# Kernel tuning notes

Measured on AMD Instinct MI355X. Metric: run time of the kernel, lower is better.

Reference implementation:

```python
import jax, jax.numpy as jnp
import numpy as np

B, H, W, D, C, K, ITERS = 16, 64, 64, 64, 16, 5, 4
EPS_LN = 1e-5

def _ln(x, g, b):
    m = x.mean(-1, keepdims=True)
    v = jnp.mean((x - m) ** 2, axis=-1, keepdims=True)
    return (x - m) / jnp.sqrt(v + EPS_LN) * g + b

def _build_grid(h, w):
    # (h, w, 2) with x in [-1,1] over width, y in [-1,1] over height
    y, x = jnp.meshgrid(jnp.linspace(-1.0, 1.0, h), jnp.linspace(-1.0, 1.0, w), indexing='ij')
    return jnp.stack([x, y], axis=-1)

def _forward(feat, feat_color, mask, slot_noise, slots_mu, slots_logsigma,
             w_grid, b_grid, w_k, w_v, ln_kv_g, ln_kv_b, w_mlp, b_mlp,
             ln_q_g, ln_q_b, w_q, w_ih, w_hh, b_ih, b_hh,
             ln_feat_g, ln_feat_b, ln_color_g, ln_color_b,
             ln_res_g, ln_res_b, w_res, b_res):
    b, h, w, d = feat.shape
    n = h * w
    k_slots = mask.shape[0]
    scale = d ** (-0.5)

    grid = _build_grid(h, w)  # (H, W, 2)

    # fg position: weighted mean of grid under mask -> (K, 2), broadcast to (B, K, 2)
    gm = grid.transpose(2, 0, 1)[None] * mask            # (K, 2, H, W)
    fg_pos = gm.sum((2, 3)) / (mask.sum((2, 3)) + 1e-5)  # (K, 2)
    fg_pos = jnp.broadcast_to(fg_pos[None], (b, k_slots, 2))

    feat_n = _ln(feat.reshape(b, n, d), ln_feat_g, ln_feat_b)                    # (B, N, D)
    featc_n = _ln(feat_color.reshape(b, n, feat_color.shape[-1]), ln_color_g, ln_color_b)

    slot = slots_mu + jnp.exp(slots_logsigma) * slot_noise  # (B, K, D)

    # k/v with relative positional grid embedding (fg_pos is constant across iters,
    # so k/v are iteration-invariant and computed once -- same math as the original loop)
    rel = grid[None, None] - fg_pos[:, :, None, None, :]        # (B, K, H, W, 2)
    rel4 = jnp.concatenate([rel, -rel], -1).reshape(b, k_slots, n, 4)
    grid_embed = rel4 @ w_grid.T + b_grid                       # (B, K, N, D)
    k = _ln(feat_n @ w_k.T[None] [0][None][0][None][0] if False else (feat_n @ w_k.T)[:, None] + grid_embed, ln_kv_g, ln_kv_b) @ w_mlp.T + b_mlp
    v = _ln((feat_n @ w_v.T)[:, None] + grid_embed, ln_kv_g, ln_kv_b) @ w_mlp.T + b_mlp

    attn = None
    for it in range(ITERS):
        prev = slot
        q = _ln(slot, ln_q_g, ln_q_b) @ w_q.T                         # (B, K, D)
        logits = jnp.einsum('bkd,bknd->bkn', q, k) * scale
        attn = jax.nn.softmax(logits, axis=-1)                        # (B, K, N)
        upd = jnp.einsum('bkn,bknd->bkd', attn, v)                    # (B, K, D)
        if it != ITERS - 1:
            # torch GRUCell
            x = upd.reshape(-1, d)
            hp = slot.reshape(-1, d)
            gi = x @ w_ih.T + b_ih
            gh = hp @ w_hh.T + b_hh
            i_r, i_z, i_n = jnp.split(gi, 3, axis=-1)
            h_r, h_z, h_n = jnp.split(gh, 3, axis=-1)
            r = jax.nn.sigmoid(i_r + h_r)
            z = jax.nn.sigmoid(i_z + h_z)
            nn_ = jnp.tanh(i_n + r * h_n)
            slot = ((1.0 - z) * nn_ + z * hp).reshape(b, k_slots, d)
            slot = _ln(slot, ln_res_g, ln_res_b) @ w_res.T + b_res + prev
        else:
            slot_color = jnp.einsum('bkn,bnc->bkc', attn, featc_n)
            slot = jnp.concatenate([slot, slot_color], axis=-1)       # (B, K, D+C)

    amin = attn.min(axis=2, keepdims=True)
    amax = attn.max(axis=2, keepdims=True)
    attn = (attn - amin) / (amax - amin + 1e-5)
    return slot, fg_pos, attn

def setup_inputs() -> dict:
    key = jax.random.key(0)
    ks = jax.random.split(key, 16)
    def rn(i, shape, s=0.02):
        return jax.random.normal(ks[i], shape, jnp.float32) * s
    return {
        'feat': jax.random.normal(ks[0], (B, H, W, D), jnp.float32),
        'feat_color': jax.random.normal(ks[1], (B, H, W, C), jnp.float32),
        'mask': jax.random.uniform(ks[2], (K, 1, H, W), jnp.float32),
        'slot_noise': jax.random.normal(ks[3], (B, K, D), jnp.float32),
        'slots_mu': rn(4, (1, 1, D), 1.0),
        'slots_logsigma': rn(5, (1, 1, D), 0.01),
        'w_grid': rn(6, (D, 4)), 'b_grid': jnp.zeros((D,), jnp.float32),
        'w_k': rn(7, (D, D)), 'w_v': rn(8, (D, D)),
        'ln_kv_g': jnp.ones((D,), jnp.float32), 'ln_kv_b': jnp.zeros((D,), jnp.float32),
        'w_mlp': rn(9, (D, D)), 'b_mlp': jnp.zeros((D,), jnp.float32),
        'ln_q_g': jnp.ones((D,), jnp.float32), 'ln_q_b': jnp.zeros((D,), jnp.float32),
        'w_q': rn(10, (D, D)),
        'w_ih': rn(11, (3 * D, D)), 'w_hh': rn(12, (3 * D, D)),
        'b_ih': jnp.zeros((3 * D,), jnp.float32), 'b_hh': jnp.zeros((3 * D,), jnp.float32),
        'ln_feat_g': jnp.ones((D,), jnp.float32), 'ln_feat_b': jnp.zeros((D,), jnp.float32),
        'ln_color_g': jnp.ones((C,), jnp.float32), 'ln_color_b': jnp.zeros((C,), jnp.float32),
        'ln_res_g': jnp.ones((D,), jnp.float32), 'ln_res_b': jnp.zeros((D,), jnp.float32),
        'w_res': rn(13, (D, D)), 'b_res': jnp.zeros((D,), jnp.float32),
    }

def reference(feat, feat_color, mask, slot_noise, slots_mu, slots_logsigma,
              w_grid, b_grid, w_k, w_v, ln_kv_g, ln_kv_b, w_mlp, b_mlp,
              ln_q_g, ln_q_b, w_q, w_ih, w_hh, b_ih, b_hh,
              ln_feat_g, ln_feat_b, ln_color_g, ln_color_b,
              ln_res_g, ln_res_b, w_res, b_res):
    return _forward(feat, feat_color, mask, slot_noise, slots_mu, slots_logsigma,
                    w_grid, b_grid, w_k, w_v, ln_kv_g, ln_kv_b, w_mlp, b_mlp,
                    ln_q_g, ln_q_b, w_q, w_ih, w_hh, b_ih, b_hh,
                    ln_feat_g, ln_feat_b, ln_color_g, ln_color_b,
                    ln_res_g, ln_res_b, w_res, b_res)
```

## Files before the change

kernel.cpp:

```cpp
#include <hip/hip_runtime.h>
#include <stdint.h>

#define B_ 16
#define H_ 64
#define W_ 64
#define D_ 64
#define C_ 16
#define K_ 5
#define N_ 4096
#define NC_ 16
#define CS_ 256
#define EPS 1e-5f

typedef __attribute__((ext_vector_type(8))) short bf16x8;
typedef __attribute__((ext_vector_type(4))) float f32x4;

__device__ __forceinline__ float wsum64(float v){
  #pragma unroll
  for(int o=1;o<64;o<<=1) v += __shfl_xor(v,o,64);
  return v;
}
__device__ __forceinline__ float wmax64(float v){
  #pragma unroll
  for(int o=1;o<64;o<<=1) v = fmaxf(v, __shfl_xor(v,o,64));
  return v;
}
__device__ __forceinline__ float wmin64(float v){
  #pragma unroll
  for(int o=1;o<64;o<<=1) v = fminf(v, __shfl_xor(v,o,64));
  return v;
}
__device__ __forceinline__ uint16_t f2bf(float f){
  uint32_t u = __float_as_uint(f);
  u += 0x7fffu + ((u>>16)&1u);
  return (uint16_t)(u>>16);
}

__global__ __launch_bounds__(256) void k_pre(
    const float* __restrict__ mask, const float* __restrict__ noise,
    const float* __restrict__ mu, const float* __restrict__ lsg,
    const float* __restrict__ wm, const float* __restrict__ bm, const float* __restrict__ lnkb,
    const float* __restrict__ wk, const float* __restrict__ wv, const float* __restrict__ lnfb,
    const float* __restrict__ wq, const float* __restrict__ lnqg, const float* __restrict__ lnqb,
    const float* __restrict__ wres, const float* __restrict__ bres,
    const float* __restrict__ lnrg, const float* __restrict__ lnrb,
    const float* __restrict__ wih, const float* __restrict__ whh,
    const float* __restrict__ wg, const float* __restrict__ bg,
    float* __restrict__ ws_fg, float* __restrict__ out_fg,
    float* __restrict__ bm2, float* __restrict__ fkb, float* __restrict__ fvb,
    float* __restrict__ qb, float* __restrict__ br2,
    float* __restrict__ wgx, float* __restrict__ wgy, float* __restrict__ gscal,
    float* __restrict__ wqpT, float* __restrict__ wrpT,
    float* __restrict__ wvT, float* __restrict__ wmT,
    float* __restrict__ gw, float* __restrict__ slot){
  int bid=blockIdx.x, tid=threadIdx.x;
  if(bid<5){
    int k=bid;
    float sm=0.f, sx=0.f, sy=0.f;
    for(int p=tid; p<H_*W_; p+=256){
      int i=p>>6, j=p&63;
      float m = mask[k*H_*W_ + p];
      float x = -1.f + (2.f/63.f)*j;
      float y = -1.f + (2.f/63.f)*i;
      sm+=m; sx+=m*x; sy+=m*y;
    }
    __shared__ float r0[4], r1[4], r2[4];
    int wid=tid>>6, lane=tid&63;
    sm=wsum64(sm); sx=wsum64(sx); sy=wsum64(sy);
    if(lane==0){ r0[wid]=sm; r1[wid]=sx; r2[wid]=sy; }
    __syncthreads();
    if(tid==0){
      float tm=r0[0]+r0[1]+r0[2]+r0[3];
      float tx=r1[0]+r1[1]+r1[2]+r1[3];
      float ty=r2[0]+r2[1]+r2[2]+r2[3];
      float px = tx/(tm+1e-5f), py = ty/(tm+1e-5f);
      ws_fg[k*2+0]=px; ws_fg[k*2+1]=py;
      for(int b=0;b<B_;b++){ out_fg[(b*K_+k)*2+0]=px; out_fg[(b*K_+k)*2+1]=py; }
    }
  } else if(bid==5){
    int sel=tid>>6, o=tid&63; float s=0.f;
    if(sel==0){ s=bm[o]; for(int d=0;d<64;d++) s+=lnkb[d]*wm[o*64+d]; bm2[o]=s; }
    else if(sel==1){ for(int d=0;d<64;d++) s+=lnqb[d]*wq[o*64+d]; qb[o]=0.125f*s; }
    else if(sel==2){ for(int d=0;d<64;d++) s+=lnrb[d]*wres[o*64+d]; br2[o]=s+bres[o]; }
    else { for(int d=0;d<64;d++) s+=lnfb[d]*wk[o*64+d]; fkb[o]=s; }
  } else if(bid==6){
    int wv4=tid>>6, l=tid&63;
    if(wv4==0){ float s=0.f; for(int d=0;d<64;d++) s+=lnfb[d]*wv[l*64+d]; fvb[l]=s; }
    else if(wv4==1){
      float4 w4 = *(const float4*)(wg + l*4);
      wgx[l]=w4.x-w4.z; wgy[l]=w4.y-w4.w;
    } else if(wv4==2){
      float4 w4 = *(const float4*)(wg + l*4);
      float wx=w4.x-w4.z, wy=w4.y-w4.w, bl=bg[l];
      float t;
      t=wsum64(wx);    if(l==0) gscal[0]=t*(1.f/64.f);
      t=wsum64(wy);    if(l==0) gscal[1]=t*(1.f/64.f);
      t=wsum64(bl);    if(l==0) gscal[2]=t*(1.f/64.f);
      t=wsum64(wx*wx); if(l==0) gscal[3]=t*(1.f/64.f);
      t=wsum64(wy*wy); if(l==0) gscal[4]=t*(1.f/64.f);
      t=wsum64(wx*wy); if(l==0) gscal[5]=t*(2.f/64.f);
      t=wsum64(wx*bl); if(l==0) gscal[6]=t*(2.f/64.f);
      t=wsum64(wy*bl); if(l==0) gscal[7]=t*(2.f/64.f);
      t=wsum64(bl*bl); if(l==0) gscal[8]=t*(1.f/64.f);
    }
  } else if(bid<71){
    int i=(bid-7)*256+tid;
    int a=i>>12, r=i&4095, d=r>>6, o=r&63;
    if(a==0)      wqpT[r]=0.125f*lnqg[d]*wq[o*64+d];
    else if(a==1) wrpT[r]=lnrg[d]*wres[o*64+d];
    else if(a==2) wvT[r]=wv[o*64+d];
    else          wmT[r]=wm[o*64+d];
  } else if(bid<167){
    int i=(bid-71)*256+tid;
    int g6=i>>12, r=i&4095, d=r>>6, o=r&63;
    float v = (g6<3)? wih[(g6*64+o)*64+d] : whh[((g6-3)*64+o)*64+d];
    gw[g6*4096 + d*64 + o] = v;
  } else {
    int i=(bid-167)*256+tid;
    if(i<B_*K_*D_){ int d=i&63; slot[i]=mu[d]+expf(lsg[d])*noise[i]; }
  }
}

__global__ __launch_bounds__(256) void k_featln(const float* __restrict__ feat,
    const float* __restrict__ wk, const float* __restrict__ wv, const float* __restrict__ gf,
    const float* __restrict__ fkb, const float* __restrict__ fvb,
    const float* __restrict__ wgx, const float* __restrict__ wgy, const float* __restrict__ bg,
    const float* __restrict__ fc, const float* __restrict__ gc, const float* __restrict__ bc,
    uint16_t* __restrict__ Aout, float4* __restrict__ kstat, float4* __restrict__ vstat,
    float* __restrict__ fcn){
  int tid=threadIdx.x, wid=tid>>6, lane=tid&63;
  int q=lane>>4, c=lane&15;
  size_t row = (size_t)blockIdx.x*64 + wid*16 + c;
  const float* xp = feat + row*64;
  float x[16];
  *(float4*)&x[0]  = *(const float4*)(xp + q*8);
  *(float4*)&x[4]  = *(const float4*)(xp + q*8 + 4);
  *(float4*)&x[8]  = *(const float4*)(xp + 32 + q*8);
  *(float4*)&x[12] = *(const float4*)(xp + 36 + q*8);
  float s=0.f;
  #pragma unroll
  for(int i=0;i<16;i++) s+=x[i];
  s += __shfl_xor(s,16,64); s += __shfl_xor(s,32,64);
  float mean = s*(1.f/64.f);
  float v=0.f;
  #pragma unroll
  for(int i=0;i<16;i++){ float d=x[i]-mean; v+=d*d; }
  v += __shfl_xor(v,16,64); v += __shfl_xor(v,32,64);
  float rs = rsqrtf(v*(1.f/64.f)+EPS);
  float gl[16];
  *(float4*)&gl[0]  = *(const float4*)(gf + q*8);
  *(float4*)&gl[4]  = *(const float4*)(gf + q*8 + 4);
  *(float4*)&gl[8]  = *(const float4*)(gf + 32 + q*8);
  *(float4*)&gl[12] = *(const float4*)(gf + 36 + q*8);
  bf16x8 A0, A1;
  #pragma unroll
  for(int j=0;j<8;j++){
    A0[j] = (short)f2bf((x[j]  -mean)*rs);
    A1[j] = (short)f2bf((x[8+j]-mean)*rs);
  }
  *(bf16x8*)(Aout + row*64 + q*8) = A0;
  *(bf16x8*)(Aout + row*64 + 32 + q*8) = A1;
  float wgxl[4][4], wgyl[4][4], bgl[4][4];
  #pragma unroll
  for(int ot=0;ot<4;ot++){
    *(float4*)&wgxl[ot][0] = *(const float4*)(wgx + ot*16 + q*4);
    *(float4*)&wgyl[ot][0] = *(const float4*)(wgy + ot*16 + q*4);
    *(float4*)&bgl[ot][0]  = *(const float4*)(bg + ot*16 + q*4);
  }
  #pragma unroll
  for(int mat=0;mat<2;mat++){
    const float* w = mat? wv : wk;
    const float* fb = mat? fvb : fkb;
    float ss=0.f, s2=0.f, dx=0.f, dy=0.f, db=0.f;
    #pragma unroll
    for(int ot=0; ot<4; ot++){
      const float* wp = w + (size_t)(ot*16+c)*64 + q*8;
      bf16x8 W0, W1;
      #pragma unroll
      for(int j=0;j<8;j++){ W0[j]=(short)f2bf(wp[j]*gl[j]); W1[j]=(short)f2bf(wp[32+j]*gl[8+j]); }
      float4 bq = *(const float4*)(fb + ot*16 + q*4);
      f32x4 acc = {bq.x,bq.y,bq.z,bq.w};
      acc = __builtin_amdgcn_mfma_f32_16x16x32_bf16(W0, A0, acc, 0,0,0);
      acc = __builtin_amdgcn_mfma_f32_16x16x32_bf16(W1, A1, acc, 0,0,0);
      #pragma unroll
      for(int r=0;r<4;r++){
        float a=acc[r];
        ss+=a; s2+=a*a;
        dx = fmaf(a, wgxl[ot][r], dx);
        dy = fmaf(a, wgyl[ot][r], dy);
        db = fmaf(a, bgl[ot][r], db);
      }
    }
    ss += __shfl_xor(ss,16,64); ss += __shfl_xor(ss,32,64);
    s2 += __shfl_xor(s2,16,64); s2 += __shfl_xor(s2,32,64);
    dx += __shfl_xor(dx,16,64); dx += __shfl_xor(dx,32,64);
    dy += __shfl_xor(dy,16,64); dy += __shfl_xor(dy,32,64);
    db += __shfl_xor(db,16,64); db += __shfl_xor(db,32,64);
    if(lane<16){
      size_t row2 = (size_t)blockIdx.x*64 + wid*16 + lane;
      float4 st = { ss*(1.f/64.f), s2*(1.f/64.f)+db*(1.f/32.f), dx*(1.f/32.f), dy*(1.f/32.f) };
      (mat? vstat : kstat)[row2] = st;
    }
  }
  int r16=tid>>4, cc=tid&15;
  #pragma unroll
  for(int i=0;i<4;i++){
    size_t row2 = (size_t)blockIdx.x*64 + i*16 + r16;
    float xv = fc[row2*16+cc];
    float sc=xv;
    #pragma unroll
    for(int o=1;o<16;o<<=1) sc += __shfl_xor(sc,o,16);
    float m2 = sc*(1.f/16.f);
    float df = xv-m2;
    float v2 = df*df;
    #pragma unroll
    for(int o=1;o<16;o<<=1) v2 += __shfl_xor(v2,o,16);
    fcn[row2*16+cc] = df*rsqrtf(v2*(1.f/16.f)+EPS)*gc[cc] + bc[cc];
  }
}

template<bool GRU>
__global__ __launch_bounds__(256) void k_slotq(
    const float* __restrict__ slot_prev, float* __restrict__ slot_cur,
    const float* __restrict__ part, const float* __restrict__ pscal,
    const float* __restrict__ red_in,
    const float* __restrict__ gw,
    const float* __restrict__ bih, const float* __restrict__ bhh,
    const float* __restrict__ wrpT, const float* __restrict__ br2,
    const float* __restrict__ wqpT, const float* __restrict__ qb,
    const float* __restrict__ wm, const float* __restrict__ wk,
    const float* __restrict__ lnfg, const float* __restrict__ lnkg,
    const float* __restrict__ fkb, const float* __restrict__ bm2, const float* __restrict__ fvb,
    const float* __restrict__ wvT, const float* __restrict__ wmT,
    const float* __restrict__ wgx, const float* __restrict__ wgy, const float* __restrict__ bg,
    const float* __restrict__ gscal,
    float* __restrict__ qs_out, float* __restrict__ cst_out){
  __shared__ float vv[64], vh[64];
  __shared__ float red6[4][64][6];
  int bk=blockIdx.x;
  int tid=threadIdx.x, wid=tid>>6, lane=tid&63;
  int o=lane, qq=wid;
  float mwgx=gscal[0], mwgy=gscal[1], mbg=gscal[2];

  #define MV(Wptr) { float p_=0.f; \
      _Pragma("unroll") \
      for(int dd=0;dd<16;dd++) p_ = fmaf(vv[qq*16+dd], (Wptr)[(qq*16+dd)*64+o], p_); \
      red6[qq][o][0]=p_; } __syncthreads();
  #define SUM0 (red6[0][lane][0]+red6[1][lane][0]+red6[2][lane][0]+red6[3][lane][0])

  float cur=0.f, qv=0.f, qp=0.f, hp=0.f;
  if(GRU){
    float As=0.f, Ax=0.f, Ay=0.f, Am=0.f;
    if(wid==0){
      float mred[NC_], sred[NC_];
      #pragma unroll
      for(int cc=0;cc<NC_;cc++){
        const float* rp = red_in + ((size_t)bk*NC_+cc)*4;
        mred[cc]=rp[0]; sred[cc]=rp[1];
      }
      float M=-1e30f;
      #pragma unroll
      for(int cc=0;cc<NC_;cc++) M=fmaxf(M,mred[cc]);
      float S=0.f;
      #pragma unroll
      for(int cc=0;cc<NC_;cc++){ mred[cc]=__expf(mred[cc]-M); S=fmaf(sred[cc],mred[cc],S); }
      float invS=1.f/S;
      float sA=0.f;
      #pragma unroll
      for(int cc=0;cc<NC_;cc++){
        float lam = mred[cc]*invS;
        sA = fmaf(lam, part[((size_t)bk*NC_+cc)*64+lane], sA);
        const float* pp = pscal + ((size_t)bk*NC_+cc)*4;
        As=fmaf(lam,pp[0],As); Ax=fmaf(lam,pp[1],Ax);
        Ay=fmaf(lam,pp[2],Ay); Am=fmaf(lam,pp[3],Am);
      }
      vv[lane] = lnfg[lane]*sA;
    }
    __syncthreads();
    MV(wvT);
    if(wid==0){
      float fvs = SUM0 + fvb[lane]*As;
      float zs = fvs + Ax*wgx[lane] + Ay*wgy[lane] + As*bg[lane] - Am;
      vv[lane] = lnkg[lane]*zs;
    }
    __syncthreads();
    MV(wmT);
    if(wid==0){
      float x_ = SUM0 + bm2[lane];
      hp = slot_prev[bk*64+lane];
      vv[lane]=x_; vh[lane]=hp;
    }
    __syncthreads();
    {
      float p0=0.f,p1=0.f,p2=0.f,p3=0.f,p4=0.f,p5=0.f;
      #pragma unroll
      for(int dd=0;dd<16;dd++){
        int d = qq*16+dd;
        float xd=vv[d], hd=vh[d];
        p0 = fmaf(xd, gw[d*64+o], p0);
        p1 = fmaf(xd, gw[4096+d*64+o], p1);
        p2 = fmaf(xd, gw[8192+d*64+o], p2);
        p3 = fmaf(hd, gw[12288+d*64+o], p3);
        p4 = fmaf(hd, gw[16384+d*64+o], p4);
        p5 = fmaf(hd, gw[20480+d*64+o], p5);
      }
      red6[qq][o][0]=p0; red6[qq][o][1]=p1; red6[qq][o][2]=p2;
      red6[qq][o][3]=p3; red6[qq][o][4]=p4; red6[qq][o][5]=p5;
    }
    __syncthreads();
    if(wid==0){
      float gir=bih[lane], giz=bih[64+lane], gin=bih[128+lane];
      float ghr=bhh[lane], ghz=bhh[64+lane], ghn=bhh[128+lane];
      #pragma unroll
      for(int w=0;w<4;w++){
        gir+=red6[w][lane][0]; giz+=red6[w][lane][1]; gin+=red6[w][lane][2];
        ghr+=red6[w][lane][3]; ghz+=red6[w][lane][4]; ghn+=red6[w][lane][5];
      }
      float r=1.f/(1.f+__expf(-(gir+ghr)));
      float z=1.f/(1.f+__expf(-(giz+ghz)));
      float nn=tanhf(gin+r*ghn);
      float sp=(1.f-z)*nn+z*hp;
      float m=wsum64(sp)*(1.f/64.f); float df=sp-m;
      float var=wsum64(df*df)*(1.f/64.f);
      vv[lane]=df*rsqrtf(var+EPS);
    }
    __syncthreads();
    MV(wrpT);
    if(wid==0){
      cur = SUM0 + br2[lane] + hp;
      slot_cur[bk*64+lane]=cur;
    }
  } else {
    if(wid==0) cur = slot_prev[bk*64+lane];
  }
  __syncthreads();
  if(wid==0){
    float m=wsum64(cur)*(1.f/64.f); float df=cur-m;
    float var=wsum64(df*df)*(1.f/64.f);
    vv[lane]=df*rsqrtf(var+EPS);
  }
  __syncthreads();
  MV(wqpT);
  if(wid==0){ qv = SUM0 + qb[lane]; vv[lane]=qv; }
  __syncthreads();
  MV(wm);
  if(wid==0){ qp = SUM0*lnkg[lane]; vv[lane]=qp; }
  __syncthreads();
  MV(wk);
  if(wid==0){
    qs_out[bk*64+lane] = SUM0*lnfg[lane];
    float s1 = wsum64(qp);
    float c1 = wsum64(qp*wgx[lane]);
    float c2 = wsum64(qp*wgy[lane]);
    float c3 = wsum64(qp*(bg[lane]+fkb[lane]));
    float c4c = wsum64(qv*bm2[lane]);
    if(lane==0){
      float* cp = cst_out + bk*8;
      cp[0]=c1-s1*mwgx; cp[1]=c2-s1*mwgy; cp[2]=c3-s1*mbg; cp[3]=s1; cp[4]=c4c;
    }
  }
  #undef MV
  #undef SUM0
}

template<bool FINAL>
__global__ __launch_bounds__(256) void k_attn(const uint16_t* __restrict__ Aw,
    const float4* __restrict__ kstat, const float4* __restrict__ vstat,
    const float* __restrict__ qsg, const float* __restrict__ cstg,
    const float* __restrict__ gscal, const float* __restrict__ ws_fg,
    float* __restrict__ lgt, float* __restrict__ red_out,
    float* __restrict__ part_o, float* __restrict__ pscal_o){
  __shared__ uint32_t As_[CS_*32];
  __shared__ float dps[5][CS_+1];
  __shared__ float pw[4][5][64];
  __shared__ float rm[4], rn[4];
  __shared__ float rsc[4][5];
  __shared__ float cstl[5][5];
  __shared__ float fgl[5][2];
  int chunk=blockIdx.x, b=blockIdx.y;
  int tid=threadIdx.x, wid=tid>>6, lane=tid&63;
  int c=lane&15, q=lane>>4;
  float mwgx=gscal[0], mwgy=gscal[1], mbg=gscal[2];
  float g1=gscal[3], g2=gscal[4], g3=gscal[5], g4=gscal[6], g5=gscal[7], g6=gscal[8];

  const uint4* Ag = (const uint4*)(Aw + ((size_t)b*N_ + chunk*CS_)*64);
  #pragma unroll
  for(int jj=0;jj<8;jj++){
    int f = jj*256 + tid;
    uint4 u = Ag[f];
    *(uint4*)(As_ + f*4) = u;
  }
  if(tid<25) cstl[tid/5][tid%5] = cstg[(b*K_ + tid/5)*8 + (tid%5)];
  if(tid>=32 && tid<42){ int i2=tid-32; fgl[i2>>1][i2&1] = ws_fg[i2]; }
  __syncthreads();

  {
    bf16x8 QF0={0,0,0,0,0,0,0,0}, QF1={0,0,0,0,0,0,0,0};
    if(c<5){
      const float* qpp = qsg + (b*K_+c)*64;
      #pragma unroll
      for(int j=0;j<8;j++){
        QF0[j] = (short)f2bf(qpp[q*8+j]);
        QF1[j] = (short)f2bf(qpp[32+q*8+j]);
      }
    }
    const uint16_t* Abase = Aw + ((size_t)b*N_ + chunk*CS_)*64;
    #pragma unroll
    for(int it=0;it<4;it++){
      int tile = wid*64 + it*16;
      const uint16_t* rp = Abase + (size_t)(tile+c)*64;
      bf16x8 BF0 = *(const bf16x8*)(rp + q*8);
      bf16x8 BF1 = *(const bf16x8*)(rp + 32 + q*8);
      f32x4 acc = {0.f,0.f,0.f,0.f};
      acc = __builtin_amdgcn_mfma_f32_16x16x32_bf16(QF0, BF0, acc, 0,0,0);
      acc = __builtin_amdgcn_mfma_f32_16x16x32_bf16(QF1, BF1, acc, 0,0,0);
      #pragma unroll
      for(int r=0;r<4;r++){
        int s = q*4+r;
        if(s<5) dps[s][tile+c]=acc[r];
      }
    }
  }
  __syncthreads();

  int t = tid;
  int n = chunk*CS_ + t;
  float4 st = kstat[(size_t)b*N_ + n];
  float4 sv;
  if(!FINAL) sv = vstat[(size_t)b*N_ + n];
  float gx = -1.f + (2.f/63.f)*(n&63);
  float gy = -1.f + (2.f/63.f)*(n>>6);
  #pragma unroll
  for(int k=0;k<5;k++){
    float rx = gx - fgl[k][0], ry = gy - fgl[k][1];
    float CX=cstl[k][0], CY=cstl[k][1], C0=cstl[k][2], S1=cstl[k][3], C4=cstl[k][4];
    float quad = g1*rx*rx + g2*ry*ry + g3*rx*ry + g4*rx + g5*ry + g6;
    float mu = st.x + rx*mwgx + ry*mwgy + mbg;
    float var = st.y + rx*st.z + ry*st.w + quad - mu*mu;
    float rsn = rsqrtf(var+EPS);
    float l = rsn*(dps[k][t] + rx*CX + ry*CY + C0 - S1*st.x) + C4;
    float wmx = wmax64(l);
    if(lane==0) rm[wid]=wmx;
    if(FINAL){ float mn=wmin64(l); if(lane==0) rn[wid]=mn; }
    __syncthreads();
    float m_c = fmaxf(fmaxf(rm[0],rm[1]),fmaxf(rm[2],rm[3]));
    float e = __expf(l-m_c);
    float scq=e, As2=0.f, Ax2=0.f, Ay2=0.f, Am2=0.f, w_=0.f;
    if(!FINAL){
      float muV = sv.x + rx*mwgx + ry*mwgy + mbg;
      float varV = sv.y + rx*sv.z + ry*sv.w + quad - muV*muV;
      float rsv_ = rsqrtf(varV+EPS);
      w_ = e*rsv_;
      As2=w_; Ax2=w_*rx; Ay2=w_*ry; Am2=w_*muV;
    } else {
      lgt[(size_t)(b*K_+k)*N_ + n] = l;
    }
    scq=wsum64(scq);
    if(!FINAL){ As2=wsum64(As2); Ax2=wsum64(Ax2); Ay2=wsum64(Ay2); Am2=wsum64(Am2); }
    if(lane==0){ rsc[wid][0]=scq; rsc[wid][1]=As2; rsc[wid][2]=Ax2; rsc[wid][3]=Ay2; rsc[wid][4]=Am2; }
    __syncthreads();
    if(tid==0){
      size_t idx = ((size_t)(b*K_+k)*NC_+chunk)*4;
      red_out[idx+0]=m_c;
      red_out[idx+1]=rsc[0][0]+rsc[1][0]+rsc[2][0]+rsc[3][0];
      if(FINAL) red_out[idx+2]=fminf(fminf(rn[0],rn[1]),fminf(rn[2],rn[3]));
      if(!FINAL){
        pscal_o[idx+0]=rsc[0][1]+rsc[1][1]+rsc[2][1]+rsc[3][1];
        pscal_o[idx+1]=rsc[0][2]+rsc[1][2]+rsc[2][2]+rsc[3][2];
        pscal_o[idx+2]=rsc[0][3]+rsc[1][3]+rsc[2][3]+rsc[3][3];
        pscal_o[idx+3]=rsc[0][4]+rsc[1][4]+rsc[2][4]+rsc[3][4];
      }
    }
    if(!FINAL) dps[k][t]=w_;
  }

  if(!FINAL){
    __syncthreads();
    const uint16_t* Au = (const uint16_t*)As_;
    float a[5]={0.f,0.f,0.f,0.f,0.f};
    for(int r64=0;r64<64;r64++){
      int row = wid*64 + r64;
      float av = __uint_as_float(((uint32_t)Au[row*64+lane])<<16);
      #pragma unroll
      for(int k=0;k<5;k++) a[k]=fmaf(dps[k][row], av, a[k]);
    }
    #pragma unroll
    for(int k=0;k<5;k++) pw[wid][k][lane]=a[k];
    __syncthreads();
    if(tid<64){
      #pragma unroll
      for(int k=0;k<5;k++){
        float s2 = pw[0][k][tid]+pw[1][k][tid]+pw[2][k][tid]+pw[3][k][tid];
        part_o[((size_t)(b*K_+k)*NC_+chunk)*64 + tid] = s2;
      }
    }
  }
}

__global__ __launch_bounds__(256) void k_fin(const float* __restrict__ lgt,
    const float* __restrict__ red, const float* __restrict__ featc,
    float* __restrict__ partc, float* __restrict__ out_attn){
  __shared__ float psp[CS_];
  __shared__ float pcz[4][16];
  int chunk=blockIdx.x, bk=blockIdx.y, b=bk/K_;
  int tid=threadIdx.x, wid=tid>>6, lane=tid&63, sub=lane>>4, c4=lane&15;
  const float* rp = red + (size_t)bk*NC_*4;
  float M=-1e30f;
  #pragma unroll
  for(int i=0;i<NC_;i++) M = fmaxf(M, rp[i*4]);
  float S=0.f;
  #pragma unroll
  for(int i=0;i<NC_;i++) S += rp[i*4+1]*__expf(rp[i*4]-M);
  float invS = 1.f/S;
  float LMIN=1e30f;
  #pragma unroll
  for(int i=0;i<NC_;i++) LMIN=fminf(LMIN, rp[i*4+2]);
  float amin = __expf(LMIN-M)*invS;
  float dinv = 1.f/(invS - amin + 1e-5f);
  const float* lp = lgt + (size_t)bk*N_ + chunk*CS_;
  {
    float p = __expf(lp[tid]-M)*invS;
    psp[tid]=p;
    out_attn[(size_t)bk*N_ + chunk*CS_ + tid] = (p - amin)*dinv;
  }
  __syncthreads();
  const float* Fb = featc + ((size_t)b*N_ + chunk*CS_)*16;
  float ac=0.f;
  for(int t=0;t<16;t++){
    int n = wid*64 + t*4 + sub;
    ac += psp[n]*Fb[(size_t)n*16 + c4];
  }
  ac+=__shfl_xor(ac,16,64); ac+=__shfl_xor(ac,32,64);
  if(lane<16) pcz[wid][lane]=ac;
  __syncthreads();
  if(tid<16){
    partc[((size_t)bk*NC_+chunk)*16 + tid] = pcz[0][tid]+pcz[1][tid]+pcz[2][tid]+pcz[3][tid];
  }
}

__global__ __launch_bounds__(64) void k_final(const float* __restrict__ slot,
    const float* __restrict__ partc, float* __restrict__ out_slot){
  int bk=blockIdx.x, lane=threadIdx.x;
  out_slot[bk*80+lane]=slot[bk*64+lane];
  if(lane<16){
    float s=0.f;
    #pragma unroll
    for(int cch=0;cch<NC_;cch++) s += partc[((size_t)bk*NC_+cch)*16+lane];
    out_slot[bk*80+64+lane]=s;
  }
}

extern "C" void kernel_launch(void* const* d_in, const int* in_sizes, int n_in,
                              void* d_out, int out_size, void* d_ws, size_t ws_size,
                              hipStream_t stream){
  (void)in_sizes; (void)n_in; (void)out_size; (void)ws_size;
  const float* feat = (const float*)d_in[0];
  const float* featc= (const float*)d_in[1];
  const float* mask = (const float*)d_in[2];
  const float* noise= (const float*)d_in[3];
  const float* mu   = (const float*)d_in[4];
  const float* lsg  = (const float*)d_in[5];
  const float* wg   = (const float*)d_in[6];
  const float* bg   = (const float*)d_in[7];
  const float* wk   = (const float*)d_in[8];
  const float* wv   = (const float*)d_in[9];
  const float* lnkg = (const float*)d_in[10];
  const float* lnkb = (const float*)d_in[11];
  const float* wm   = (const float*)d_in[12];
  const float* bm   = (const float*)d_in[13];
  const float* lnqg = (const float*)d_in[14];
  const float* lnqb = (const float*)d_in[15];
  const float* wq   = (const float*)d_in[16];
  const float* wih  = (const float*)d_in[17];
  const float* whh  = (const float*)d_in[18];
  const float* bih  = (const float*)d_in[19];
  const float* bhh  = (const float*)d_in[20];
  const float* lnfg = (const float*)d_in[21];
  const float* lnfb = (const float*)d_in[22];
  const float* lncg = (const float*)d_in[23];
  const float* lncb = (const float*)d_in[24];
  const float* lnrg = (const float*)d_in[25];
  const float* lnrb = (const float*)d_in[26];
  const float* wres = (const float*)d_in[27];
  const float* bres = (const float*)d_in[28];

  float* out = (float*)d_out;
  float* out_slot = out;
  float* out_fg   = out + 6400;
  float* out_attn = out + 6560;

  float* wsf     = (float*)d_ws;
  float* ws_fg   = wsf;
  float* ws_bm2  = wsf + 16;
  float* ws_fkb  = ws_bm2 + 64;
  float* ws_fvb  = ws_fkb + 64;
  float* ws_qb   = ws_fvb + 64;
  float* ws_br2  = ws_qb + 64;
  float* ws_wgx  = ws_br2 + 64;
  float* ws_wgy  = ws_wgx + 64;
  float* ws_gs   = ws_wgy + 64;
  float* ws_wqpT = ws_gs + 16;
  float* ws_wrpT = ws_wqpT + 4096;
  float* ws_wvT  = ws_wrpT + 4096;
  float* ws_wmT  = ws_wvT + 4096;
  float* ws_gw   = ws_wmT + 4096;
  float* ws_fc   = ws_gw + 24576;
  float* ws_sl0  = ws_fc + (size_t)B_*N_*C_;
  float* ws_sl1  = ws_sl0 + B_*K_*D_;
  float* ws_qs   = ws_sl1 + B_*K_*D_;
  float* ws_cst  = ws_qs + B_*K_*D_;
  float* ws_lgt  = ws_cst + 640;
  float* ws_red0 = ws_lgt + (size_t)B_*K_*N_;
  float* ws_red1 = ws_red0 + B_*K_*NC_*4;
  float* ws_prt0 = ws_red1 + B_*K_*NC_*4;
  float* ws_prt1 = ws_prt0 + (size_t)B_*K_*NC_*64;
  float* ws_psc0 = ws_prt1 + (size_t)B_*K_*NC_*64;
  float* ws_psc1 = ws_psc0 + B_*K_*NC_*4;
  float* ws_pc   = ws_psc1 + B_*K_*NC_*4;
  float4* ws_kst = (float4*)(ws_pc + B_*K_*NC_*16);
  float4* ws_vst = ws_kst + (size_t)B_*N_;
  uint16_t* ws_A = (uint16_t*)(ws_vst + (size_t)B_*N_);

  k_pre<<<187,256,0,stream>>>(mask,noise,mu,lsg, wm,bm,lnkb, wk,wv,lnfb,
                              wq,lnqg,lnqb, wres,bres,lnrg,lnrb, wih,whh, wg,bg,
                              ws_fg,out_fg, ws_bm2,ws_fkb,ws_fvb,ws_qb,ws_br2,
                              ws_wgx,ws_wgy,ws_gs,
                              ws_wqpT,ws_wrpT,ws_wvT,ws_wmT, ws_gw, ws_sl0);
  k_featln<<<(B_*N_)/64,256,0,stream>>>(feat,wk,wv,lnfg,ws_fkb,ws_fvb,
                                        ws_wgx,ws_wgy,bg,
                                        featc,lncg,lncb,
                                        ws_A,ws_kst,ws_vst,ws_fc);

  dim3 agrid(NC_,B_);
  #define SQ_ARGS(SPREV,SCUR,PIN,SCIN,RIN) SPREV,SCUR,PIN,SCIN,RIN,ws_gw, \
      bih,bhh,ws_wrpT,ws_br2,ws_wqpT,ws_qb, wm,wk,lnfg,lnkg, \
      ws_fkb,ws_bm2,ws_fvb, ws_wvT,ws_wmT, ws_wgx,ws_wgy,bg, ws_gs, ws_qs,ws_cst
  #define AT_ARGS(ROUT,POUT,SCOUT) ws_A,ws_kst,ws_vst,ws_qs,ws_cst,ws_gs,ws_fg, \
      ws_lgt,ROUT,POUT,SCOUT

  k_slotq<false><<<B_*K_,256,0,stream>>>(SQ_ARGS(ws_sl0,ws_sl0,ws_prt1,ws_psc1,ws_red1));
  k_attn<false><<<agrid,256,0,stream>>>(AT_ARGS(ws_red0,ws_prt0,ws_psc0));
  k_slotq<true><<<B_*K_,256,0,stream>>>(SQ_ARGS(ws_sl0,ws_sl1,ws_prt0,ws_psc0,ws_red0));
  k_attn<false><<<agrid,256,0,stream>>>(AT_ARGS(ws_red1,ws_prt1,ws_psc1));
  k_slotq<true><<<B_*K_,256,0,stream>>>(SQ_ARGS(ws_sl1,ws_sl0,ws_prt1,ws_psc1,ws_red1));
  k_attn<false><<<agrid,256,0,stream>>>(AT_ARGS(ws_red0,ws_prt0,ws_psc0));
  k_slotq<true><<<B_*K_,256,0,stream>>>(SQ_ARGS(ws_sl0,ws_sl1,ws_prt0,ws_psc0,ws_red0));
  k_attn<true><<<agrid,256,0,stream>>>(AT_ARGS(ws_red1,ws_prt1,ws_psc1));
  k_fin<<<dim3(NC_,B_*K_),256,0,stream>>>(ws_lgt,ws_red1,ws_fc,ws_pc,out_attn);
  k_final<<<B_*K_,64,0,stream>>>(ws_sl1, ws_pc, out_slot);
}
```

Baseline: 224.0 us.

## Halve attention chunk size, batch per-slot reductions, fuse final slot output via atomics

Doubles the number of N-chunks (NC 16→32, CS 256→128) so the attention and finalize kernels launch twice as many blocks on the GPU. In k_attn only half the threads do per-row work. The five per-slot softmax reductions are batched so the kernel hits two block barriers instead of two per slot. The slot-side combine of chunk partials is spread across lanes and waves with warp reductions. k_final is removed: k_fin atomically adds the color partials into a pre-zeroed output and copies the slots, at the cost of idle threads in k_attn and nondeterministic float atomic ordering.

```diff
diff --git a/kernel.cpp b/kernel.cpp
--- a/kernel.cpp
+++ b/kernel.cpp
@@ -8,8 +8,8 @@
 #define C_ 16
 #define K_ 5
 #define N_ 4096
-#define NC_ 16
-#define CS_ 256
+#define NC_ 32
+#define CS_ 128
 #define EPS 1e-5f
 
 typedef __attribute__((ext_vector_type(8))) short bf16x8;
@@ -52,7 +52,7 @@
     float* __restrict__ wgx, float* __restrict__ wgy, float* __restrict__ gscal,
     float* __restrict__ wqpT, float* __restrict__ wrpT,
     float* __restrict__ wvT, float* __restrict__ wmT,
-    float* __restrict__ gw, float* __restrict__ slot){
+    float* __restrict__ gw, float* __restrict__ slot, float* __restrict__ out_slot){
   int bid=blockIdx.x, tid=threadIdx.x;
   if(bid<5){
     int k=bid;
@@ -102,6 +102,8 @@
       t=wsum64(wx*bl); if(l==0) gscal[6]=t*(2.f/64.f);
       t=wsum64(wy*bl); if(l==0) gscal[7]=t*(2.f/64.f);
       t=wsum64(bl*bl); if(l==0) gscal[8]=t*(1.f/64.f);
+    } else {
+      for(int j=l;j<B_*K_*16;j+=64){ int bk2=j>>4, cc2=j&15; out_slot[bk2*80+64+cc2]=0.f; }
     }
   } else if(bid<71){
     int i=(bid-7)*256+tid;
@@ -237,6 +239,7 @@
     float* __restrict__ qs_out, float* __restrict__ cst_out){
   __shared__ float vv[64], vh[64];
   __shared__ float red6[4][64][6];
+  __shared__ float lamb[NC_];
   int bk=blockIdx.x;
   int tid=threadIdx.x, wid=tid>>6, lane=tid&63;
   int o=lane, qq=wid;
@@ -252,28 +255,33 @@
   if(GRU){
     float As=0.f, Ax=0.f, Ay=0.f, Am=0.f;
     if(wid==0){
-      float mred[NC_], sred[NC_];
-      #pragma unroll
-      for(int cc=0;cc<NC_;cc++){
-        const float* rp = red_in + ((size_t)bk*NC_+cc)*4;
-        mred[cc]=rp[0]; sred[cc]=rp[1];
-      }
-      float M=-1e30f;
-      #pragma unroll
-      for(int cc=0;cc<NC_;cc++) M=fmaxf(M,mred[cc]);
-      float S=0.f;
-      #pragma unroll
-      for(int cc=0;cc<NC_;cc++){ mred[cc]=__expf(mred[cc]-M); S=fmaf(sred[cc],mred[cc],S); }
-      float invS=1.f/S;
-      float sA=0.f;
-      #pragma unroll
-      for(int cc=0;cc<NC_;cc++){
-        float lam = mred[cc]*invS;
-        sA = fmaf(lam, part[((size_t)bk*NC_+cc)*64+lane], sA);
-        const float* pp = pscal + ((size_t)bk*NC_+cc)*4;
-        As=fmaf(lam,pp[0],As); Ax=fmaf(lam,pp[1],Ax);
-        Ay=fmaf(lam,pp[2],Ay); Am=fmaf(lam,pp[3],Am);
-      }
+      float m_l = (lane<NC_)? red_in[((size_t)bk*NC_+lane)*4]   : -1e30f;
+      float s_l = (lane<NC_)? red_in[((size_t)bk*NC_+lane)*4+1] : 0.f;
+      float M = wmax64(m_l);
+      float eu = (lane<NC_)? __expf(m_l-M) : 0.f;
+      float S = wsum64(s_l*eu);
+      float lam = eu/S;
+      if(lane<NC_) lamb[lane]=lam;
+      float p0 = (lane<NC_)? pscal[((size_t)bk*NC_+lane)*4+0] : 0.f;
+      float p1 = (lane<NC_)? pscal[((size_t)bk*NC_+lane)*4+1] : 0.f;
+      float p2 = (lane<NC_)? pscal[((size_t)bk*NC_+lane)*4+2] : 0.f;
+      float p3 = (lane<NC_)? pscal[((size_t)bk*NC_+lane)*4+3] : 0.f;
+      As = wsum64(lam*p0); Ax = wsum64(lam*p1);
+      Ay = wsum64(lam*p2); Am = wsum64(lam*p3);
+    }
+    __syncthreads();
+    {
+      float p_=0.f;
+      #pragma unroll
+      for(int j=0;j<8;j++){
+        int cc = qq*8+j;
+        p_ = fmaf(lamb[cc], part[((size_t)bk*NC_+cc)*64+o], p_);
+      }
+      red6[qq][o][0]=p_;
+    }
+    __syncthreads();
+    if(wid==0){
+      float sA = SUM0;
       vv[lane] = lnfg[lane]*sA;
     }
     __syncthreads();
@@ -371,10 +379,10 @@
     float* __restrict__ lgt, float* __restrict__ red_out,
     float* __restrict__ part_o, float* __restrict__ pscal_o){
   __shared__ uint32_t As_[CS_*32];
-  __shared__ float dps[5][CS_+1];
+  __shared__ float dps[5][CS_+4];
   __shared__ float pw[4][5][64];
-  __shared__ float rm[4], rn[4];
-  __shared__ float rsc[4][5];
+  __shared__ float rm[2][5], rn[2][5];
+  __shared__ float rsc[2][5][5];
   __shared__ float cstl[5][5];
   __shared__ float fgl[5][2];
   int chunk=blockIdx.x, b=blockIdx.y;
@@ -385,13 +393,22 @@
 
   const uint4* Ag = (const uint4*)(Aw + ((size_t)b*N_ + chunk*CS_)*64);
   #pragma unroll
-  for(int jj=0;jj<8;jj++){
+  for(int jj=0;jj<4;jj++){
     int f = jj*256 + tid;
-    uint4 u = Ag[f];
-    *(uint4*)(As_ + f*4) = u;
+    *(uint4*)(As_ + f*4) = Ag[f];
   }
   if(tid<25) cstl[tid/5][tid%5] = cstg[(b*K_ + tid/5)*8 + (tid%5)];
   if(tid>=32 && tid<42){ int i2=tid-32; fgl[i2>>1][i2&1] = ws_fg[i2]; }
+  bool act = tid < CS_;
+  int nrow = chunk*CS_ + (tid & (CS_-1));
+  float4 st, sv;
+  float gx=0.f, gy=0.f;
+  if(act){
+    st = kstat[(size_t)b*N_ + nrow];
+    if(!FINAL) sv = vstat[(size_t)b*N_ + nrow];
+    gx = -1.f + (2.f/63.f)*(nrow&63);
+    gy = -1.f + (2.f/63.f)*(nrow>>6);
+  }
   __syncthreads();
 
   {
@@ -406,8 +423,8 @@
     }
     const uint16_t* Abase = Aw + ((size_t)b*N_ + chunk*CS_)*64;
     #pragma unroll
-    for(int it=0;it<4;it++){
-      int tile = wid*64 + it*16;
+    for(int it=0;it<2;it++){
+      int tile = wid*32 + it*16;
       const uint16_t* rp = Abase + (size_t)(tile+c)*64;
       bf16x8 BF0 = *(const bf16x8*)(rp + q*8);
       bf16x8 BF1 = *(const bf16x8*)(rp + 32 + q*8);
@@ -423,63 +440,72 @@
   }
   __syncthreads();
 
-  int t = tid;
-  int n = chunk*CS_ + t;
-  float4 st = kstat[(size_t)b*N_ + n];
-  float4 sv;
-  if(!FINAL) sv = vstat[(size_t)b*N_ + n];
-  float gx = -1.f + (2.f/63.f)*(n&63);
-  float gy = -1.f + (2.f/63.f)*(n>>6);
-  #pragma unroll
-  for(int k=0;k<5;k++){
-    float rx = gx - fgl[k][0], ry = gy - fgl[k][1];
-    float CX=cstl[k][0], CY=cstl[k][1], C0=cstl[k][2], S1=cstl[k][3], C4=cstl[k][4];
-    float quad = g1*rx*rx + g2*ry*ry + g3*rx*ry + g4*rx + g5*ry + g6;
-    float mu = st.x + rx*mwgx + ry*mwgy + mbg;
-    float var = st.y + rx*st.z + ry*st.w + quad - mu*mu;
-    float rsn = rsqrtf(var+EPS);
-    float l = rsn*(dps[k][t] + rx*CX + ry*CY + C0 - S1*st.x) + C4;
-    float wmx = wmax64(l);
-    if(lane==0) rm[wid]=wmx;
-    if(FINAL){ float mn=wmin64(l); if(lane==0) rn[wid]=mn; }
-    __syncthreads();
-    float m_c = fmaxf(fmaxf(rm[0],rm[1]),fmaxf(rm[2],rm[3]));
-    float e = __expf(l-m_c);
-    float scq=e, As2=0.f, Ax2=0.f, Ay2=0.f, Am2=0.f, w_=0.f;
+  float l5[5], w5[5];
+  if(act){
+    #pragma unroll
+    for(int k=0;k<5;k++){
+      float rx = gx - fgl[k][0], ry = gy - fgl[k][1];
+      float CX=cstl[k][0], CY=cstl[k][1], C0=cstl[k][2], S1=cstl[k][3], C4=cstl[k][4];
+      float quad = g1*rx*rx + g2*ry*ry + g3*rx*ry + g4*rx + g5*ry + g6;
+      float mu = st.x + rx*mwgx + ry*mwgy + mbg;
+      float var = st.y + rx*st.z + ry*st.w + quad - mu*mu;
+      float rsn = rsqrtf(var+EPS);
+      float l = rsn*(dps[k][tid] + rx*CX + ry*CY + C0 - S1*st.x) + C4;
+      l5[k]=l;
+      float wmx = wmax64(l);
+      if(lane==0) rm[wid][k]=wmx;
+      if(FINAL){ float mn=wmin64(l); if(lane==0) rn[wid][k]=mn; }
+    }
+  }
+  __syncthreads();
+  if(act){
+    #pragma unroll
+    for(int k=0;k<5;k++){
+      float m_c = fmaxf(rm[0][k], rm[1][k]);
+      float e = __expf(l5[k]-m_c);
+      float scq = wsum64(e);
+      if(!FINAL){
+        float rx = gx - fgl[k][0], ry = gy - fgl[k][1];
+        float quad = g1*rx*rx + g2*ry*ry + g3*rx*ry + g4*rx + g5*ry + g6;
+        float muV = sv.x + rx*mwgx + ry*mwgy + mbg;
+        float varV = sv.y + rx*sv.z + ry*sv.w + quad - muV*muV;
+        float rsv_ = rsqrtf(varV+EPS);
+        float w_ = e*rsv_;
+        w5[k]=w_;
+        float As2=wsum64(w_), Ax2=wsum64(w_*rx), Ay2=wsum64(w_*ry), Am2=wsum64(w_*muV);
+        if(lane==0){ rsc[wid][k][0]=scq; rsc[wid][k][1]=As2; rsc[wid][k][2]=Ax2;
+                     rsc[wid][k][3]=Ay2; rsc[wid][k][4]=Am2; }
+      } else {
+        lgt[(size_t)(b*K_+k)*N_ + nrow] = l5[k];
+        if(lane==0) rsc[wid][k][0]=scq;
+      }
+    }
+  }
+  __syncthreads();
+  if(tid<5){
+    int k=tid;
+    size_t idx = ((size_t)(b*K_+k)*NC_+chunk)*4;
+    red_out[idx+0]=fmaxf(rm[0][k],rm[1][k]);
+    red_out[idx+1]=rsc[0][k][0]+rsc[1][k][0];
+    if(FINAL) red_out[idx+2]=fminf(rn[0][k],rn[1][k]);
     if(!FINAL){
-      float muV = sv.x + rx*mwgx + ry*mwgy + mbg;
-      float varV = sv.y + rx*sv.z + ry*sv.w + quad - muV*muV;
-      float rsv_ = rsqrtf(varV+EPS);
-      w_ = e*rsv_;
-      As2=w_; Ax2=w_*rx; Ay2=w_*ry; Am2=w_*muV;
-    } else {
-      lgt[(size_t)(b*K_+k)*N_ + n] = l;
-    }
-    scq=wsum64(scq);
-    if(!FINAL){ As2=wsum64(As2); Ax2=wsum64(Ax2); Ay2=wsum64(Ay2); Am2=wsum64(Am2); }
-    if(lane==0){ rsc[wid][0]=scq; rsc[wid][1]=As2; rsc[wid][2]=Ax2; rsc[wid][3]=Ay2; rsc[wid][4]=Am2; }
-    __syncthreads();
-    if(tid==0){
-      size_t idx = ((size_t)(b*K_+k)*NC_+chunk)*4;
-      red_out[idx+0]=m_c;
-      red_out[idx+1]=rsc[0][0]+rsc[1][0]+rsc[2][0]+rsc[3][0];
-      if(FINAL) red_out[idx+2]=fminf(fminf(rn[0],rn[1]),fminf(rn[2],rn[3]));
-      if(!FINAL){
-        pscal_o[idx+0]=rsc[0][1]+rsc[1][1]+rsc[2][1]+rsc[3][1];
-        pscal_o[idx+1]=rsc[0][2]+rsc[1][2]+rsc[2][2]+rsc[3][2];
-        pscal_o[idx+2]=rsc[0][3]+rsc[1][3]+rsc[2][3]+rsc[3][3];
-        pscal_o[idx+3]=rsc[0][4]+rsc[1][4]+rsc[2][4]+rsc[3][4];
-      }
-    }
-    if(!FINAL) dps[k][t]=w_;
+      pscal_o[idx+0]=rsc[0][k][1]+rsc[1][k][1];
+      pscal_o[idx+1]=rsc[0][k][2]+rsc[1][k][2];
+      pscal_o[idx+2]=rsc[0][k][3]+rsc[1][k][3];
+      pscal_o[idx+3]=rsc[0][k][4]+rsc[1][k][4];
+    }
+  }
+  if(act && !FINAL){
+    #pragma unroll
+    for(int k=0;k<5;k++) dps[k][tid]=w5[k];
   }
 
   if(!FINAL){
     __syncthreads();
     const uint16_t* Au = (const uint16_t*)As_;
     float a[5]={0.f,0.f,0.f,0.f,0.f};
-    for(int r64=0;r64<64;r64++){
-      int row = wid*64 + r64;
+    for(int r32=0;r32<32;r32++){
+      int row = wid*32 + r32;
       float av = __uint_as_float(((uint32_t)Au[row*64+lane])<<16);
       #pragma unroll
       for(int k=0;k<5;k++) a[k]=fmaf(dps[k][row], av, a[k]);
@@ -499,7 +525,8 @@
 
 __global__ __launch_bounds__(256) void k_fin(const float* __restrict__ lgt,
     const float* __restrict__ red, const float* __restrict__ featc,
-    float* __restrict__ partc, float* __restrict__ out_attn){
+    const float* __restrict__ sl1, float* __restrict__ out_slot,
+    float* __restrict__ out_attn){
   __shared__ float psp[CS_];
   __shared__ float pcz[4][16];
   int chunk=blockIdx.x, bk=blockIdx.y, b=bk/K_;
@@ -518,7 +545,7 @@
   float amin = __expf(LMIN-M)*invS;
   float dinv = 1.f/(invS - amin + 1e-5f);
   const float* lp = lgt + (size_t)bk*N_ + chunk*CS_;
-  {
+  if(tid<CS_){
     float p = __expf(lp[tid]-M)*invS;
     psp[tid]=p;
     out_attn[(size_t)bk*N_ + chunk*CS_ + tid] = (p - amin)*dinv;
@@ -526,28 +553,18 @@
   __syncthreads();
   const float* Fb = featc + ((size_t)b*N_ + chunk*CS_)*16;
   float ac=0.f;
-  for(int t=0;t<16;t++){
-    int n = wid*64 + t*4 + sub;
+  for(int t=0;t<8;t++){
+    int n = wid*32 + t*4 + sub;
     ac += psp[n]*Fb[(size_t)n*16 + c4];
   }
   ac+=__shfl_xor(ac,16,64); ac+=__shfl_xor(ac,32,64);
   if(lane<16) pcz[wid][lane]=ac;
   __syncthreads();
   if(tid<16){
-    partc[((size_t)bk*NC_+chunk)*16 + tid] = pcz[0][tid]+pcz[1][tid]+pcz[2][tid]+pcz[3][tid];
-  }
-}
-
-__global__ __launch_bounds__(64) void k_final(const float* __restrict__ slot,
-    const float* __restrict__ partc, float* __restrict__ out_slot){
-  int bk=blockIdx.x, lane=threadIdx.x;
-  out_slot[bk*80+lane]=slot[bk*64+lane];
-  if(lane<16){
-    float s=0.f;
-    #pragma unroll
-    for(int cch=0;cch<NC_;cch++) s += partc[((size_t)bk*NC_+cch)*16+lane];
-    out_slot[bk*80+64+lane]=s;
-  }
+    float s2 = pcz[0][tid]+pcz[1][tid]+pcz[2][tid]+pcz[3][tid];
+    atomicAdd(&out_slot[bk*80+64+tid], s2);
+  }
+  if(chunk==0 && tid<64) out_slot[bk*80+tid]=sl1[bk*64+tid];
 }
 
 extern "C" void kernel_launch(void* const* d_in, const int* in_sizes, int n_in,
@@ -616,8 +633,7 @@
   float* ws_prt1 = ws_prt0 + (size_t)B_*K_*NC_*64;
   float* ws_psc0 = ws_prt1 + (size_t)B_*K_*NC_*64;
   float* ws_psc1 = ws_psc0 + B_*K_*NC_*4;
-  float* ws_pc   = ws_psc1 + B_*K_*NC_*4;
-  float4* ws_kst = (float4*)(ws_pc + B_*K_*NC_*16);
+  float4* ws_kst = (float4*)(ws_psc1 + B_*K_*NC_*4);
   float4* ws_vst = ws_kst + (size_t)B_*N_;
   uint16_t* ws_A = (uint16_t*)(ws_vst + (size_t)B_*N_);
 
@@ -625,7 +641,7 @@
                               wq,lnqg,lnqb, wres,bres,lnrg,lnrb, wih,whh, wg,bg,
                               ws_fg,out_fg, ws_bm2,ws_fkb,ws_fvb,ws_qb,ws_br2,
                               ws_wgx,ws_wgy,ws_gs,
-                              ws_wqpT,ws_wrpT,ws_wvT,ws_wmT, ws_gw, ws_sl0);
+                              ws_wqpT,ws_wrpT,ws_wvT,ws_wmT, ws_gw, ws_sl0, out_slot);
   k_featln<<<(B_*N_)/64,256,0,stream>>>(feat,wk,wv,lnfg,ws_fkb,ws_fvb,
                                         ws_wgx,ws_wgy,bg,
                                         featc,lncg,lncb,
@@ -646,6 +662,5 @@
   k_attn<false><<<agrid,256,0,stream>>>(AT_ARGS(ws_red0,ws_prt0,ws_psc0));
   k_slotq<true><<<B_*K_,256,0,stream>>>(SQ_ARGS(ws_sl0,ws_sl1,ws_prt0,ws_psc0,ws_red0));
   k_attn<true><<<agrid,256,0,stream>>>(AT_ARGS(ws_red1,ws_prt1,ws_psc1));
-  k_fin<<<dim3(NC_,B_*K_),256,0,stream>>>(ws_lgt,ws_red1,ws_fc,ws_pc,out_attn);
-  k_final<<<B_*K_,64,0,stream>>>(ws_sl1, ws_pc, out_slot);
-}
+  k_fin<<<dim3(NC_,B_*K_),256,0,stream>>>(ws_lgt,ws_red1,ws_fc,ws_sl1,out_slot,out_attn);
+}
```

Result: no change. 222.5 us (-0.7%).
